# Kernel tuning notes

Measured on AMD Instinct MI355X. Metric: run time of the kernel, lower is better.

Reference implementation:

```python
import jax, jax.numpy as jnp
import numpy as np

N_GRAPHS = 8


def glorot(key, shape):
    fan_in, fan_out = shape[0], shape[1]
    s = (6.0 / (fan_in + fan_out)) ** 0.5
    return jax.random.uniform(key, shape, jnp.float32, -s, s)


def setup_inputs() -> dict:
    key = jax.random.key(0)
    ks = jax.random.split(key, 8)
    N, E, C = 100000, 800000, 128
    x = jax.random.normal(ks[0], (N, C), jnp.float32)
    edge_index = jax.random.randint(ks[1], (2, E), 0, N, jnp.int64)
    batch = jnp.sort(jax.random.randint(ks[2], (N,), 0, N_GRAPHS, jnp.int64))
    W1 = glorot(ks[3], (C, 64));   b1 = jnp.zeros((64,), jnp.float32)
    W2 = glorot(ks[4], (64, 128)); b2 = jnp.zeros((128,), jnp.float32)
    W3 = glorot(ks[5], (128, 256)); b3 = jnp.zeros((256,), jnp.float32)
    Wfc = glorot(ks[6], (256, 1))
    bfc = jax.random.normal(ks[7], (1,), jnp.float32) * 0.01
    return {"x": x, "edge_index": edge_index, "batch": batch,
            "W1": W1, "b1": b1, "W2": W2, "b2": b2, "W3": W3, "b3": b3,
            "Wfc": Wfc, "bfc": bfc}


def _gcn_layer(h_in, W, b, src, dst, norm_edge, self_coef, n):
    # GCNConv: x' = D^{-1/2}(A+I)D^{-1/2} (x W) + b   (self-loops included)
    h = h_in @ W                                     # [N, out]
    msg = h[src] * norm_edge[:, None]                # gather + edge normalize
    agg = jax.ops.segment_sum(msg, dst, num_segments=n)  # scatter-add
    agg = agg + h * self_coef[:, None]               # self-loop contribution
    return agg + b


def reference(x, edge_index, batch, W1, b1, W2, b2, W3, b3, Wfc, bfc):
    n = x.shape[0]
    src, dst = edge_index[0], edge_index[1]
    # gcn_norm with self-loops: deg = in-degree + 1
    deg = jax.ops.segment_sum(jnp.ones_like(dst, dtype=x.dtype), dst, num_segments=n) + 1.0
    dis = deg ** -0.5
    norm_edge = dis[src] * dis[dst]
    self_coef = dis * dis
    h = jax.nn.relu(_gcn_layer(x, W1, b1, src, dst, norm_edge, self_coef, n))
    h = jax.nn.relu(_gcn_layer(h, W2, b2, src, dst, norm_edge, self_coef, n))
    h = jax.nn.relu(_gcn_layer(h, W3, b3, src, dst, norm_edge, self_coef, n))
    # global_mean_pool over graphs
    counts = jax.ops.segment_sum(jnp.ones((n,), x.dtype), batch, num_segments=N_GRAPHS)
    pooled = jax.ops.segment_sum(h, batch, num_segments=N_GRAPHS) / counts[:, None]
    return pooled @ Wfc + bfc
```

## Files before the change

kernel.cpp:

```cpp
#include <hip/hip_runtime.h>
#include <hip/hip_bf16.h>

typedef __attribute__((ext_vector_type(8))) short short8v;
typedef __attribute__((ext_vector_type(4))) float f32x4;

static __device__ __forceinline__ unsigned short f2bf(float f) {
  __hip_bfloat16 b = __float2bfloat16(f);
  return *reinterpret_cast<unsigned short*>(&b);
}
static __device__ __forceinline__ float bf2f(unsigned short u) {
  unsigned int x = ((unsigned int)u) << 16;
  return __builtin_bit_cast(float, x);
}
static __device__ __forceinline__ float bflo(unsigned int u) {
  return __builtin_bit_cast(float, u << 16);
}
static __device__ __forceinline__ float bfhi(unsigned int u) {
  return __builtin_bit_cast(float, u & 0xffff0000u);
}

__global__ __launch_bounds__(256) void k_hist(const int* __restrict__ ei,
                                              int* __restrict__ cnt, int E) {
  int stride = gridDim.x * blockDim.x;
  for (int i = blockIdx.x * blockDim.x + threadIdx.x; i < E; i += stride)
    atomicAdd(&cnt[ei[E + i]], 1);
}

__global__ __launch_bounds__(256) void k_scan1(const int* __restrict__ cnt,
                                               int* __restrict__ row_tmp,
                                               int* __restrict__ bsum, int N) {
  __shared__ int sd[256];
  const int tid = threadIdx.x;
  const int i = blockIdx.x * 256 + tid;
  int v = (i < N) ? cnt[i] : 0;
  sd[tid] = v;
  __syncthreads();
#pragma unroll
  for (int off = 1; off < 256; off <<= 1) {
    int t = (tid >= off) ? sd[tid - off] : 0;
    __syncthreads();
    sd[tid] += t;
    __syncthreads();
  }
  if (i < N) row_tmp[i] = sd[tid] - v;
  if (tid == 255) bsum[blockIdx.x] = sd[255];
}

__global__ __launch_bounds__(1024) void k_scan2(int* __restrict__ bsum, int nb) {
  __shared__ int sd[1024];
  const int t = threadIdx.x;
  int v = (t < nb) ? bsum[t] : 0;
  sd[t] = v;
  __syncthreads();
#pragma unroll
  for (int off = 1; off < 1024; off <<= 1) {
    int x = (t >= off) ? sd[t - off] : 0;
    __syncthreads();
    sd[t] += x;
    __syncthreads();
  }
  if (t < nb) bsum[t] = sd[t] - v;
}

__global__ __launch_bounds__(256) void k_scan3(const int* __restrict__ row_tmp,
                                               const int* __restrict__ bsum,
                                               const int* __restrict__ cnt,
                                               const int* __restrict__ batch,
                                               float* __restrict__ dis,
                                               int* __restrict__ row_ptr,
                                               int* __restrict__ cursor,
                                               int* __restrict__ gstart, int N,
                                               int E) {
  const int i = blockIdx.x * 256 + threadIdx.x;
  if (i < N) {
    int rp = row_tmp[i] + bsum[i >> 8];
    row_ptr[i] = rp;
    cursor[i] = rp;
    dis[i] = 1.0f / sqrtf((float)cnt[i] + 1.0f);
    int b = batch[i];
    if (i == 0) {
      for (int g = 0; g <= b; ++g) gstart[g] = 0;
    } else {
      int p = batch[i - 1];
      for (int g = p + 1; g <= b; ++g) gstart[g] = i;
    }
    if (i == N - 1)
      for (int g = b + 1; g <= 8; ++g) gstart[g] = N;
  }
  if (i == 0) row_ptr[N] = E;
}

__global__ __launch_bounds__(256) void k_fill(const int* __restrict__ ei,
                                              int* __restrict__ cursor,
                                              int* __restrict__ col, int E) {
  int stride = gridDim.x * blockDim.x;
  for (int e = blockIdx.x * blockDim.x + threadIdx.x; e < E; e += stride) {
    int s = ei[e];
    int d = ei[E + e];
    int pos = atomicAdd(&cursor[d], 1);
    col[pos] = s;
  }
}

static __device__ __forceinline__ void pack_one(const float* __restrict__ W,
                                                unsigned short* __restrict__ Wp,
                                                int K, int M, int t) {
  int KT = K >> 5;
  int lane = t & 63;
  int tile = t >> 6;
  int kt = tile % KT;
  int ct = tile / KT;
  int c = ct * 16 + (lane & 15);
  int k0 = kt * 32 + (lane >> 4) * 8;
  unsigned short v[8];
#pragma unroll
  for (int j = 0; j < 8; ++j) v[j] = f2bf(W[(size_t)(k0 + j) * M + c]);
  ushort4* dst = (ushort4*)&Wp[(size_t)t * 8];
  dst[0] = make_ushort4(v[0], v[1], v[2], v[3]);
  dst[1] = make_ushort4(v[4], v[5], v[6], v[7]);
}

__global__ __launch_bounds__(256) void k_packall(
    const float* __restrict__ W1, const float* __restrict__ W2,
    const float* __restrict__ W3, unsigned short* __restrict__ Wp1,
    unsigned short* __restrict__ Wp2, unsigned short* __restrict__ Wp3) {
  int t = blockIdx.x * 256 + threadIdx.x;
  if (t < 1024)
    pack_one(W1, Wp1, 128, 64, t);
  else if (t < 2048)
    pack_one(W2, Wp2, 64, 128, t - 1024);
  else if (t < 6144)
    pack_one(W3, Wp3, 128, 256, t - 2048);
}

template <bool EPI>
__global__ __launch_bounds__(256) void k_agg64(const int* __restrict__ row_ptr,
                                               const int* __restrict__ col,
                                               const float* __restrict__ dis,
                                               const unsigned short* __restrict__ Hin,
                                               const float* __restrict__ bias,
                                               unsigned short* __restrict__ Pout,
                                               int N) {
  const int lane = threadIdx.x & 63;
  int d = blockIdx.x * 4 + (threadIdx.x >> 6);
  if (d >= N) return;
  const int q = lane >> 3;
  const int cl = lane & 7;
  const int cb = cl * 8;
  const float disd = dis[d];
  const int beg = row_ptr[d];
  const int end = row_ptr[d + 1];
  const int deg = end - beg;
  const int nedge = min(deg, 64);

  int s_l = d;
  float w_l = 0.f;
  if (lane < nedge) {
    s_l = col[beg + lane];
    w_l = dis[s_l] * disd;
  }

  float acc[8];
#pragma unroll
  for (int k = 0; k < 8; ++k) acc[k] = 0.f;
  if (q == 0) {
    uint4 u = *(const uint4*)&Hin[(size_t)d * 64 + cb];
    const float sc = disd * disd;
    acc[0] = bflo(u.x) * sc; acc[1] = bfhi(u.x) * sc;
    acc[2] = bflo(u.y) * sc; acc[3] = bfhi(u.y) * sc;
    acc[4] = bflo(u.z) * sc; acc[5] = bfhi(u.z) * sc;
    acc[6] = bflo(u.w) * sc; acc[7] = bfhi(u.w) * sc;
  }

  const int padded = (nedge + 15) & ~15;
  for (int base = 0; base < padded; base += 16) {
    int e0 = base + q, e1 = base + 8 + q;
    int s0 = __shfl(s_l, e0, 64);
    float w0 = __shfl(w_l, e0, 64);
    int s1 = __shfl(s_l, e1, 64);
    float w1 = __shfl(w_l, e1, 64);
    if (e0 >= nedge) { s0 = d; w0 = 0.f; }
    if (e1 >= nedge) { s1 = d; w1 = 0.f; }
    uint4 u0 = *(const uint4*)&Hin[(size_t)s0 * 64 + cb];
    uint4 u1 = *(const uint4*)&Hin[(size_t)s1 * 64 + cb];
    acc[0] = fmaf(bflo(u0.x), w0, acc[0]); acc[1] = fmaf(bfhi(u0.x), w0, acc[1]);
    acc[2] = fmaf(bflo(u0.y), w0, acc[2]); acc[3] = fmaf(bfhi(u0.y), w0, acc[3]);
    acc[4] = fmaf(bflo(u0.z), w0, acc[4]); acc[5] = fmaf(bfhi(u0.z), w0, acc[5]);
    acc[6] = fmaf(bflo(u0.w), w0, acc[6]); acc[7] = fmaf(bfhi(u0.w), w0, acc[7]);
    acc[0] = fmaf(bflo(u1.x), w1, acc[0]); acc[1] = fmaf(bfhi(u1.x), w1, acc[1]);
    acc[2] = fmaf(bflo(u1.y), w1, acc[2]); acc[3] = fmaf(bfhi(u1.y), w1, acc[3]);
    acc[4] = fmaf(bflo(u1.z), w1, acc[4]); acc[5] = fmaf(bfhi(u1.z), w1, acc[5]);
    acc[6] = fmaf(bflo(u1.w), w1, acc[6]); acc[7] = fmaf(bfhi(u1.w), w1, acc[7]);
  }
  if (deg > 64) {
    for (int j = beg + 64 + q; j < end; j += 8) {
      int s = col[j];
      float w = dis[s] * disd;
      uint4 u = *(const uint4*)&Hin[(size_t)s * 64 + cb];
      acc[0] = fmaf(bflo(u.x), w, acc[0]); acc[1] = fmaf(bfhi(u.x), w, acc[1]);
      acc[2] = fmaf(bflo(u.y), w, acc[2]); acc[3] = fmaf(bfhi(u.y), w, acc[3]);
      acc[4] = fmaf(bflo(u.z), w, acc[4]); acc[5] = fmaf(bfhi(u.z), w, acc[5]);
      acc[6] = fmaf(bflo(u.w), w, acc[6]); acc[7] = fmaf(bfhi(u.w), w, acc[7]);
    }
  }

#pragma unroll
  for (int k = 0; k < 8; ++k) {
    acc[k] += __shfl_xor(acc[k], 8, 64);
    acc[k] += __shfl_xor(acc[k], 16, 64);
    acc[k] += __shfl_xor(acc[k], 32, 64);
  }
  if (q == 0) {
    if (EPI) {
#pragma unroll
      for (int k = 0; k < 8; ++k) acc[k] = fmaxf(acc[k] + bias[cb + k], 0.f);
    }
    uint4 o;
    o.x = (unsigned)f2bf(acc[0]) | ((unsigned)f2bf(acc[1]) << 16);
    o.y = (unsigned)f2bf(acc[2]) | ((unsigned)f2bf(acc[3]) << 16);
    o.z = (unsigned)f2bf(acc[4]) | ((unsigned)f2bf(acc[5]) << 16);
    o.w = (unsigned)f2bf(acc[6]) | ((unsigned)f2bf(acc[7]) << 16);
    *(uint4*)&Pout[(size_t)d * 64 + cb] = o;
  }
}

__global__ __launch_bounds__(256) void k_agg128(const int* __restrict__ row_ptr,
                                                const int* __restrict__ col,
                                                const float* __restrict__ dis,
                                                const unsigned short* __restrict__ Hin,
                                                unsigned short* __restrict__ Pout,
                                                int N) {
  const int lane = threadIdx.x & 63;
  int d = blockIdx.x * 4 + (threadIdx.x >> 6);
  if (d >= N) return;
  const int q = lane >> 4;
  const int cl = lane & 15;
  const int cb = cl * 8;
  const float disd = dis[d];
  const int beg = row_ptr[d];
  const int end = row_ptr[d + 1];
  const int deg = end - beg;
  const int nedge = min(deg, 64);

  int s_l = d;
  float w_l = 0.f;
  if (lane < nedge) {
    s_l = col[beg + lane];
    w_l = dis[s_l] * disd;
  }

  float acc[8];
#pragma unroll
  for (int k = 0; k < 8; ++k) acc[k] = 0.f;
  if (q == 0) {
    uint4 u = *(const uint4*)&Hin[(size_t)d * 128 + cb];
    const float sc = disd * disd;
    acc[0] = bflo(u.x) * sc; acc[1] = bfhi(u.x) * sc;
    acc[2] = bflo(u.y) * sc; acc[3] = bfhi(u.y) * sc;
    acc[4] = bflo(u.z) * sc; acc[5] = bfhi(u.z) * sc;
    acc[6] = bflo(u.w) * sc; acc[7] = bfhi(u.w) * sc;
  }

  const int padded = (nedge + 7) & ~7;
  for (int base = 0; base < padded; base += 8) {
    int e0 = base + q, e1 = base + 4 + q;
    int s0 = __shfl(s_l, e0, 64);
    float w0 = __shfl(w_l, e0, 64);
    int s1 = __shfl(s_l, e1, 64);
    float w1 = __shfl(w_l, e1, 64);
    if (e0 >= nedge) { s0 = d; w0 = 0.f; }
    if (e1 >= nedge) { s1 = d; w1 = 0.f; }
    uint4 u0 = *(const uint4*)&Hin[(size_t)s0 * 128 + cb];
    uint4 u1 = *(const uint4*)&Hin[(size_t)s1 * 128 + cb];
    acc[0] = fmaf(bflo(u0.x), w0, acc[0]); acc[1] = fmaf(bfhi(u0.x), w0, acc[1]);
    acc[2] = fmaf(bflo(u0.y), w0, acc[2]); acc[3] = fmaf(bfhi(u0.y), w0, acc[3]);
    acc[4] = fmaf(bflo(u0.z), w0, acc[4]); acc[5] = fmaf(bfhi(u0.z), w0, acc[5]);
    acc[6] = fmaf(bflo(u0.w), w0, acc[6]); acc[7] = fmaf(bfhi(u0.w), w0, acc[7]);
    acc[0] = fmaf(bflo(u1.x), w1, acc[0]); acc[1] = fmaf(bfhi(u1.x), w1, acc[1]);
    acc[2] = fmaf(bflo(u1.y), w1, acc[2]); acc[3] = fmaf(bfhi(u1.y), w1, acc[3]);
    acc[4] = fmaf(bflo(u1.z), w1, acc[4]); acc[5] = fmaf(bfhi(u1.z), w1, acc[5]);
    acc[6] = fmaf(bflo(u1.w), w1, acc[6]); acc[7] = fmaf(bfhi(u1.w), w1, acc[7]);
  }
  if (deg > 64) {
    for (int j = beg + 64 + q; j < end; j += 4) {
      int s = col[j];
      float w = dis[s] * disd;
      uint4 u = *(const uint4*)&Hin[(size_t)s * 128 + cb];
      acc[0] = fmaf(bflo(u.x), w, acc[0]); acc[1] = fmaf(bfhi(u.x), w, acc[1]);
      acc[2] = fmaf(bflo(u.y), w, acc[2]); acc[3] = fmaf(bfhi(u.y), w, acc[3]);
      acc[4] = fmaf(bflo(u.z), w, acc[4]); acc[5] = fmaf(bfhi(u.z), w, acc[5]);
      acc[6] = fmaf(bflo(u.w), w, acc[6]); acc[7] = fmaf(bfhi(u.w), w, acc[7]);
    }
  }

#pragma unroll
  for (int k = 0; k < 8; ++k) {
    acc[k] += __shfl_xor(acc[k], 16, 64);
    acc[k] += __shfl_xor(acc[k], 32, 64);
  }
  if (q == 0) {
    uint4 o;
    o.x = (unsigned)f2bf(acc[0]) | ((unsigned)f2bf(acc[1]) << 16);
    o.y = (unsigned)f2bf(acc[2]) | ((unsigned)f2bf(acc[3]) << 16);
    o.z = (unsigned)f2bf(acc[4]) | ((unsigned)f2bf(acc[5]) << 16);
    o.w = (unsigned)f2bf(acc[6]) | ((unsigned)f2bf(acc[7]) << 16);
    *(uint4*)&Pout[(size_t)d * 128 + cb] = o;
  }
}

template <int K, int M, bool F32IN, bool BIAS>
__global__ __launch_bounds__(256) void k_mm(const void* __restrict__ Ap,
                                            const unsigned short* __restrict__ Wp,
                                            const float* __restrict__ bias,
                                            unsigned short* __restrict__ Hout,
                                            int N) {
  constexpr int KT = K / 32, CT = M / 16;
  const int lane = threadIdx.x & 63;
  const int wid = threadIdx.x >> 6;
  int row0 = (blockIdx.x * 4 + wid) * 16;
  row0 = __builtin_amdgcn_readfirstlane(row0);
  if (row0 >= N) return;
  const int r = lane & 15;
  const int kh = lane >> 4;

  int arow = row0 + r;
  if (arow >= N) arow = N - 1;

  f32x4 acc[CT];
#pragma unroll
  for (int ct = 0; ct < CT; ++ct) acc[ct] = (f32x4){0.f, 0.f, 0.f, 0.f};

#pragma unroll
  for (int kt = 0; kt < KT; ++kt) {
    short8v a;
    if (F32IN) {
      const float* Af = (const float*)Ap;
      const float* p = &Af[(size_t)arow * K + kt * 32 + kh * 8];
      float4 f0 = *(const float4*)p;
      float4 f1 = *(const float4*)(p + 4);
      a[0] = (short)f2bf(f0.x); a[1] = (short)f2bf(f0.y);
      a[2] = (short)f2bf(f0.z); a[3] = (short)f2bf(f0.w);
      a[4] = (short)f2bf(f1.x); a[5] = (short)f2bf(f1.y);
      a[6] = (short)f2bf(f1.z); a[7] = (short)f2bf(f1.w);
    } else {
      const unsigned short* Ab = (const unsigned short*)Ap;
      a = *(const short8v*)&Ab[(size_t)arow * K + kt * 32 + kh * 8];
    }
#pragma unroll
    for (int ct = 0; ct < CT; ++ct) {
      short8v b = *(const short8v*)&Wp[(size_t)((ct * KT + kt) * 64 + lane) * 8];
      acc[ct] = __builtin_amdgcn_mfma_f32_16x16x32_bf16(a, b, acc[ct], 0, 0, 0);
    }
  }

  const int orow0 = row0 + kh * 4;
#pragma unroll
  for (int ct = 0; ct < CT; ++ct) {
    const int c = ct * 16 + r;
    const float bv = BIAS ? bias[c] : 0.f;
#pragma unroll
    for (int reg = 0; reg < 4; ++reg) {
      int row = orow0 + reg;
      if (row < N) {
        float v = acc[ct][reg] + bv;
        if (BIAS) v = fmaxf(v, 0.f);
        Hout[(size_t)row * M + c] = f2bf(v);
      }
    }
  }
}

__global__ __launch_bounds__(256) void k_pool2(const unsigned short* __restrict__ H4,
                                               const int* __restrict__ gstart,
                                               float* __restrict__ pooled) {
  __shared__ float sd[8][256];
  const int g = blockIdx.y;
  const int s = gstart[g], e = gstart[g + 1];
  if (s >= e) return;
  const int PB = gridDim.x;
  const int chunk = (e - s + PB - 1) / PB;
  const int r0 = s + blockIdx.x * chunk;
  const int r1 = min(e, r0 + chunk);

  const int t = threadIdx.x;
  const int rs = t >> 5;
  const int cl = t & 31;
  const int cb = cl * 8;

  float a[8];
#pragma unroll
  for (int k = 0; k < 8; ++k) a[k] = 0.f;

  for (int r = r0 + rs; r < r1; r += 8) {
    uint4 u = *(const uint4*)&H4[(size_t)r * 256 + cb];
    a[0] += bflo(u.x); a[1] += bfhi(u.x);
    a[2] += bflo(u.y); a[3] += bfhi(u.y);
    a[4] += bflo(u.z); a[5] += bfhi(u.z);
    a[6] += bflo(u.w); a[7] += bfhi(u.w);
  }
#pragma unroll
  for (int k = 0; k < 8; ++k) sd[rs][cb + k] = a[k];
  __syncthreads();
  float v = 0.f;
#pragma unroll
  for (int q = 0; q < 8; ++q) v += sd[q][t];
  atomicAdd(&pooled[g * 256 + t], v);
}

__global__ __launch_bounds__(256) void k_final(const float* __restrict__ pooled,
                                               const int* __restrict__ gstart,
                                               const float* __restrict__ Wfc,
                                               const float* __restrict__ bfc,
                                               float* __restrict__ out) {
  __shared__ float red[4];
  const int t = threadIdx.x;
  for (int g = 0; g < 8; ++g) {
    float cg = (float)(gstart[g + 1] - gstart[g]);
    float v = pooled[g * 256 + t] / cg * Wfc[t];
#pragma unroll
    for (int off = 32; off > 0; off >>= 1) v += __shfl_down(v, off, 64);
    if ((t & 63) == 0) red[t >> 6] = v;
    __syncthreads();
    if (t == 0) out[g] = red[0] + red[1] + red[2] + red[3] + bfc[0];
    __syncthreads();
  }
}

extern "C" void kernel_launch(void* const* d_in, const int* in_sizes, int n_in,
                              void* d_out, int out_size, void* d_ws,
                              size_t ws_size, hipStream_t stream) {
  const float* x = (const float*)d_in[0];
  const int* ei = (const int*)d_in[1];
  const int* batch = (const int*)d_in[2];
  const float* W1 = (const float*)d_in[3];
  const float* b1 = (const float*)d_in[4];
  const float* W2 = (const float*)d_in[5];
  const float* b2 = (const float*)d_in[6];
  const float* W3 = (const float*)d_in[7];
  const float* b3 = (const float*)d_in[8];
  const float* Wfc = (const float*)d_in[9];
  const float* bfc = (const float*)d_in[10];
  float* out = (float*)d_out;

  const int N = in_sizes[0] / 128;
  const int E = in_sizes[1] / 2;
  const int nb = (N + 255) / 256;

  float* ws = (float*)d_ws;
  size_t o = 0;
  float* dis = ws + o;            o += (size_t)N;
  int* cnt = (int*)(ws + o);      o += (size_t)N;
  int* row_tmp = (int*)(ws + o);  o += (size_t)N;
  int* bsum = (int*)(ws + o);     o += 1024;
  int* row_ptr = (int*)(ws + o);  o += (size_t)N + 1;
  int* cursor = (int*)(ws + o);   o += (size_t)N;
  int* col = (int*)(ws + o);      o += (size_t)E;
  float* pooled = ws + o;         o += 2048;
  int* gstart = (int*)(ws + o);   o += 16;
  unsigned short* Wp1 = (unsigned short*)(ws + o); o += 4096;
  unsigned short* Wp2 = (unsigned short*)(ws + o); o += 4096;
  unsigned short* Wp3 = (unsigned short*)(ws + o); o += 16384;
  o = (o + 63) & ~(size_t)63;
  unsigned short* bufA = (unsigned short*)(ws + o); o += (size_t)N * 32;
  unsigned short* bufB = (unsigned short*)(ws + o); o += (size_t)N * 32;
  unsigned short* bufC = (unsigned short*)(ws + o); o += (size_t)N * 64;
  unsigned short* bufD = (unsigned short*)(ws + o); o += (size_t)N * 64;
  unsigned short* bufE = (unsigned short*)(ws + o); o += (size_t)N * 128;

  hipMemsetAsync(cnt, 0, (size_t)N * sizeof(int), stream);
  hipMemsetAsync(pooled, 0, 2048 * sizeof(float), stream);

  k_hist<<<2048, 256, 0, stream>>>(ei, cnt, E);
  k_scan1<<<nb, 256, 0, stream>>>(cnt, row_tmp, bsum, N);
  k_scan2<<<1, 1024, 0, stream>>>(bsum, nb);
  k_scan3<<<nb, 256, 0, stream>>>(row_tmp, bsum, cnt, batch, dis, row_ptr,
                                  cursor, gstart, N, E);
  k_fill<<<2048, 256, 0, stream>>>(ei, cursor, col, E);
  k_packall<<<24, 256, 0, stream>>>(W1, W2, W3, Wp1, Wp2, Wp3);

  const int ablocks = (N + 3) / 4;
  const int mblocks = (N + 63) / 64;
  k_mm<128, 64, true, false><<<mblocks, 256, 0, stream>>>(x, Wp1, nullptr, bufA, N);
  k_agg64<true><<<ablocks, 256, 0, stream>>>(row_ptr, col, dis, bufA, b1, bufB, N);
  k_agg64<false><<<ablocks, 256, 0, stream>>>(row_ptr, col, dis, bufB, nullptr, bufA, N);
  k_mm<64, 128, false, true><<<mblocks, 256, 0, stream>>>(bufA, Wp2, b2, bufC, N);
  k_agg128<<<ablocks, 256, 0, stream>>>(row_ptr, col, dis, bufC, bufD, N);
  k_mm<128, 256, false, true><<<mblocks, 256, 0, stream>>>(bufD, Wp3, b3, bufE, N);

  k_pool2<<<dim3(128, 8), 256, 0, stream>>>(bufE, gstart, pooled);
  k_final<<<1, 256, 0, stream>>>(pooled, gstart, Wfc, bfc, out);
}
```

Before: 420.6 us.

## Build CSR via two-level bucketed scatter instead of per-node global atomics

Replaces the single-pass CSR fill, which did one global atomicAdd per edge on per-node cursors, with a two-pass bucketed approach. Edges are first scattered into 256-node buckets using shared-memory ranking and one global atomic per bucket per block. A second kernel then places each bucket's edges into final column positions using shared-memory atomics. The aim is to cut global atomic contention and improve write locality, at the cost of an extra pass and an intermediate pairs buffer of E uint2 entries.

```diff
diff --git a/kernel.cpp b/kernel.cpp
--- a/kernel.cpp
+++ b/kernel.cpp
@@ -68,14 +68,14 @@
                                                const int* __restrict__ batch,
                                                float* __restrict__ dis,
                                                int* __restrict__ row_ptr,
-                                               int* __restrict__ cursor,
+                                               int* __restrict__ bucket_cur,
                                                int* __restrict__ gstart, int N,
                                                int E) {
   const int i = blockIdx.x * 256 + threadIdx.x;
   if (i < N) {
     int rp = row_tmp[i] + bsum[i >> 8];
     row_ptr[i] = rp;
-    cursor[i] = rp;
+    if ((i & 255) == 0) bucket_cur[i >> 8] = rp;
     dis[i] = 1.0f / sqrtf((float)cnt[i] + 1.0f);
     int b = batch[i];
     if (i == 0) {
@@ -90,15 +90,52 @@
   if (i == 0) row_ptr[N] = E;
 }
 
-__global__ __launch_bounds__(256) void k_fill(const int* __restrict__ ei,
-                                              int* __restrict__ cursor,
-                                              int* __restrict__ col, int E) {
-  int stride = gridDim.x * blockDim.x;
-  for (int e = blockIdx.x * blockDim.x + threadIdx.x; e < E; e += stride) {
-    int s = ei[e];
-    int d = ei[E + e];
-    int pos = atomicAdd(&cursor[d], 1);
-    col[pos] = s;
+__global__ __launch_bounds__(256) void k_b3(const int* __restrict__ ei,
+                                            int* __restrict__ bucket_cur,
+                                            uint2* __restrict__ pairs, int E) {
+  __shared__ int cntD[512];
+  __shared__ int gbase[512];
+  const int t = threadIdx.x;
+  for (int i = t; i < 512; i += 256) cntD[i] = 0;
+  __syncthreads();
+  const int base = blockIdx.x * 2048;
+  int s[8], d[8], rk[8];
+#pragma unroll
+  for (int i = 0; i < 8; ++i) {
+    int e = base + i * 256 + t;
+    if (e < E) {
+      s[i] = ei[e];
+      d[i] = ei[E + e];
+      rk[i] = atomicAdd(&cntD[d[i] >> 8], 1);
+    }
+  }
+  __syncthreads();
+  for (int i = t; i < 512; i += 256)
+    if (cntD[i] > 0) gbase[i] = atomicAdd(&bucket_cur[i], cntD[i]);
+  __syncthreads();
+#pragma unroll
+  for (int i = 0; i < 8; ++i) {
+    int e = base + i * 256 + t;
+    if (e < E)
+      pairs[gbase[d[i] >> 8] + rk[i]] = make_uint2((unsigned)s[i], (unsigned)d[i]);
+  }
+}
+
+__global__ __launch_bounds__(256) void k_b4(const int* __restrict__ row_ptr,
+                                            const uint2* __restrict__ pairs,
+                                            int* __restrict__ col, int N) {
+  __shared__ int curL[257];
+  const int n0 = blockIdx.x << 8;
+  const int nn = min(256, N - n0);
+  const int t = threadIdx.x;
+  for (int i = t; i <= nn; i += 256) curL[i] = row_ptr[n0 + i];
+  __syncthreads();
+  const int p0 = curL[0], p1 = curL[nn];
+  __syncthreads();
+  for (int idx = p0 + t; idx < p1; idx += 256) {
+    uint2 pr = pairs[idx];
+    int pos = atomicAdd(&curL[(int)pr.y - n0], 1);
+    col[pos] = (int)pr.x;
   }
 }
 
@@ -445,6 +482,7 @@
   const int N = in_sizes[0] / 128;
   const int E = in_sizes[1] / 2;
   const int nb = (N + 255) / 256;
+  const int nbk = (N + 255) >> 8;
 
   float* ws = (float*)d_ws;
   size_t o = 0;
@@ -453,8 +491,9 @@
   int* row_tmp = (int*)(ws + o);  o += (size_t)N;
   int* bsum = (int*)(ws + o);     o += 1024;
   int* row_ptr = (int*)(ws + o);  o += (size_t)N + 1;
-  int* cursor = (int*)(ws + o);   o += (size_t)N;
+  int* bucket_cur = (int*)(ws + o); o += 512;
   int* col = (int*)(ws + o);      o += (size_t)E;
+  uint2* pairs = (uint2*)(ws + o); o += (size_t)E * 2;
   float* pooled = ws + o;         o += 2048;
   int* gstart = (int*)(ws + o);   o += 16;
   unsigned short* Wp1 = (unsigned short*)(ws + o); o += 4096;
@@ -474,8 +513,9 @@
   k_scan1<<<nb, 256, 0, stream>>>(cnt, row_tmp, bsum, N);
   k_scan2<<<1, 1024, 0, stream>>>(bsum, nb);
   k_scan3<<<nb, 256, 0, stream>>>(row_tmp, bsum, cnt, batch, dis, row_ptr,
-                                  cursor, gstart, N, E);
-  k_fill<<<2048, 256, 0, stream>>>(ei, cursor, col, E);
+                                  bucket_cur, gstart, N, E);
+  k_b3<<<(E + 2047) / 2048, 256, 0, stream>>>(ei, bucket_cur, pairs, E);
+  k_b4<<<nbk, 256, 0, stream>>>(row_ptr, pairs, col, N);
   k_packall<<<24, 256, 0, stream>>>(W1, W2, W3, Wp1, Wp2, Wp3);
 
   const int ablocks = (N + 3) / 4;
```

Result: faster. 391.2 us (-7.0%).
